# Optimization experiments

Measured on AMD Instinct MI355X. Metric: run time of the kernel, lower is better.

## Reference

```python
import jax, jax.numpy as jnp
import numpy as np

EPS = 1e-15
SCALING = 2.0  # softmax scaling in AttentionReference.forward default


def _psd(xs, mask):
    """ESPnet get_power_spectral_density_matrix with fused einsum.
    xs:   (B, F, C, T) complex64
    mask: (B, F, C, T) float32
    returns psd: (B, F, C, C) complex64
    """
    m = mask.mean(axis=-2)                               # (B, F, T)
    m = m / (m.sum(axis=-1, keepdims=True) + EPS)        # normalize over T
    # fused masked covariance: sum_t m[t] * x[:,t] x[:,t]^H
    return jnp.einsum('bfct,bft,bfet->bfce', xs, m.astype(xs.dtype), jnp.conj(xs))


def _attention_reference(psd_in, mlp_w, mlp_b, gvec_w, gvec_b):
    """AttentionReference.forward. psd_in: (B,F,C,C) complex -> u: (B,C)."""
    C = psd_in.shape[-1]
    eye = jnp.eye(C, dtype=bool)
    psd = jnp.where(eye, jnp.zeros((), psd_in.dtype), psd_in)   # zero diagonal
    psd = jnp.swapaxes(psd.sum(axis=-1) / (C - 1), -1, -2)      # (B, C, F)
    psd_feat = jnp.sqrt(psd.real ** 2 + psd.imag ** 2)          # (B, C, F)
    mlp = jnp.tanh(psd_feat @ mlp_w + mlp_b)                    # (B, C, A)
    e = (mlp @ gvec_w + gvec_b)[..., 0]                         # (B, C)
    return jax.nn.softmax(SCALING * e, axis=-1)                 # (B, C)


def _mvdr_vector(psd_s, psd_n, u):
    """get_mvdr_vector: ws = inv(psd_n) @ psd_s / trace(.) then contract with u."""
    numerator = jnp.linalg.inv(psd_n) @ psd_s                   # (B, F, C, C)
    trace = jnp.einsum('bfcc->bf', numerator)
    ws_mat = numerator / (trace[..., None, None] + EPS)
    return jnp.einsum('bfec,bc->bfe', ws_mat, u.astype(ws_mat.dtype))  # (B, F, C)


def setup_inputs() -> dict:
    key = jax.random.key(0)
    ks = jax.random.split(key, 6)
    B, T, C, F, A = 8, 512, 8, 257, 320
    return {
        'data_real': jax.random.normal(ks[0], (B, T, C, F), jnp.float32),
        'data_imag': jax.random.normal(ks[1], (B, T, C, F), jnp.float32),
        'mask_speech': jax.random.uniform(ks[2], (B, F, C, T), jnp.float32),
        'mask_noise': jax.random.uniform(ks[3], (B, F, C, T), jnp.float32),
        'mlp_w': jax.random.normal(ks[4], (F, A), jnp.float32) / np.sqrt(F),
        'mlp_b': jnp.zeros((A,), jnp.float32),
        'gvec_w': jax.random.normal(ks[5], (A, 1), jnp.float32) / np.sqrt(A),
        'gvec_b': jnp.zeros((1,), jnp.float32),
        'ilens': jnp.full((B,), T, dtype=jnp.int32),
    }


def reference(data_real, data_imag, mask_speech, mask_noise,
              mlp_w, mlp_b, gvec_w, gvec_b, ilens):
    # data: (B,T,C,F) -> permute(0,3,2,1) -> (B,F,C,T)
    data = jnp.transpose(data_real + 1j * data_imag, (0, 3, 2, 1)).astype(jnp.complex64)
    psd_speech = _psd(data, mask_speech)    # (B,F,C,C)
    psd_noise = _psd(data, mask_noise)      # (B,F,C,C)
    u = _attention_reference(psd_speech, mlp_w, mlp_b, gvec_w, gvec_b)  # (B,C)
    ws = _mvdr_vector(psd_speech, psd_noise, u)                         # (B,F,C)
    # apply_beamforming_vector: conj(ws) . data over channels -> (B,F,T)
    enhanced = jnp.einsum('bfc,bfct->bft', jnp.conj(ws), data)
    enhanced = jnp.swapaxes(enhanced, -1, -2)                           # (B,T,F)
    # complex output packed as real (B,T,F,2)
    return jnp.stack([enhanced.real, enhanced.imag], axis=-1)
```

## Files before the change

### kernel.cpp

```cpp
#include <hip/hip_runtime.h>
#include <math.h>

#define TTOT 512
#define CCH 8
#define FFR 257
#define AAH 320
#define NBF 2056
#define BF2 2112
#define NTIL 16
#define TTILE 32
#define EPSF 1e-15f
#define WSB (FFR * 8)

#define OFF_MBS 0
#define OFF_MBN (OFF_MBS + NBF * 512)
#define OFF_PART (OFF_MBN + NBF * 512)
#define OFF_PSDS (OFF_PART + NTIL * 256 * BF2)
#define OFF_PSDN (OFF_PSDS + NBF * 128)
#define OFF_E (OFF_PSDN + NBF * 128)
#define OFF_WS (OFF_E + 64)

__global__ __launch_bounds__(256) void k_mask(
    const float* __restrict__ mask_s, const float* __restrict__ mask_n,
    float* __restrict__ mbar_s, float* __restrict__ mbar_n) {
  int bf = blockIdx.x;
  int tid = threadIdx.x;
  int lane = tid & 63, wv = tid >> 6;
  const float2* ms = (const float2*)(mask_s + (size_t)bf * CCH * TTOT);
  const float2* mn = (const float2*)(mask_n + (size_t)bf * CCH * TTOT);
  float2 ss = make_float2(0.f, 0.f), sn = make_float2(0.f, 0.f);
#pragma unroll
  for (int c = 0; c < 8; ++c) {
    float2 a = ms[c * 256 + tid];
    ss.x += a.x; ss.y += a.y;
    float2 b = mn[c * 256 + tid];
    sn.x += b.x; sn.y += b.y;
  }
  float tots = ss.x + ss.y, totn = sn.x + sn.y;
#pragma unroll
  for (int off = 32; off > 0; off >>= 1) {
    tots += __shfl_down(tots, off);
    totn += __shfl_down(totn, off);
  }
  __shared__ float reds[4], redn[4];
  if (lane == 0) { reds[wv] = tots; redn[wv] = totn; }
  __syncthreads();
  float totS = reds[0] + reds[1] + reds[2] + reds[3];
  float totN = redn[0] + redn[1] + redn[2] + redn[3];
  float invs = 0.125f / (totS * 0.125f + EPSF);
  float invn = 0.125f / (totN * 0.125f + EPSF);
  ((float2*)(mbar_s + (size_t)bf * TTOT))[tid] = make_float2(ss.x * invs, ss.y * invs);
  ((float2*)(mbar_n + (size_t)bf * TTOT))[tid] = make_float2(sn.x * invn, sn.y * invn);
}

__global__ __launch_bounds__(256) void k_psd(
    const float* __restrict__ dr, const float* __restrict__ di,
    const float* __restrict__ mbar_s, const float* __restrict__ mbar_n,
    float* __restrict__ partial) {
  int lane = threadIdx.x & 63, wv = threadIdx.x >> 6;
  int bfb = blockIdx.x;
  int ttile = blockIdx.y;
  int bf = bfb * 64 + lane;
  if (bf > NBF - 1) bf = NBF - 1;
  int b = bf / FFR, f = bf - b * FFR;
  size_t dbase = (size_t)b * TTOT * CCH * FFR + f;
  int qi = (wv >> 1) * 4, qj = (wv & 1) * 4;
  bool diag = (qi == qj);
  int t0 = ttile * TTILE;

  float acc[16][4];
#pragma unroll
  for (int p = 0; p < 16; ++p) {
    acc[p][0] = 0.f; acc[p][1] = 0.f; acc[p][2] = 0.f; acc[p][3] = 0.f;
  }

#pragma unroll 2
  for (int tt = 0; tt < TTILE; ++tt) {
    int t = t0 + tt;
    const float* pr = dr + dbase + (size_t)t * (CCH * FFR);
    const float* pim_ = di + dbase + (size_t)t * (CCH * FFR);
    float ir[4], ii[4], jr[4], ji[4];
#pragma unroll
    for (int k = 0; k < 4; ++k) {
      ir[k] = pr[(qi + k) * FFR];
      ii[k] = pim_[(qi + k) * FFR];
    }
    if (!diag) {
#pragma unroll
      for (int k = 0; k < 4; ++k) {
        jr[k] = pr[(qj + k) * FFR];
        ji[k] = pim_[(qj + k) * FFR];
      }
    } else {
#pragma unroll
      for (int k = 0; k < 4; ++k) { jr[k] = ir[k]; ji[k] = ii[k]; }
    }
    float m_s = mbar_s[(size_t)bf * TTOT + t];
    float m_n = mbar_n[(size_t)bf * TTOT + t];
#pragma unroll
    for (int i4 = 0; i4 < 4; ++i4)
#pragma unroll
      for (int j4 = 0; j4 < 4; ++j4) {
        int p = i4 * 4 + j4;
        float pre = ir[i4] * jr[j4] + ii[i4] * ji[j4];
        float pimv = ii[i4] * jr[j4] - ir[i4] * ji[j4];
        acc[p][0] += m_s * pre; acc[p][1] += m_s * pimv;
        acc[p][2] += m_n * pre; acc[p][3] += m_n * pimv;
      }
  }

  size_t pbase = (size_t)ttile * 256 * BF2 + (size_t)wv * 64 * BF2 + bfb * 64 + lane;
#pragma unroll
  for (int p = 0; p < 16; ++p)
#pragma unroll
    for (int comp = 0; comp < 4; ++comp)
      partial[pbase + (size_t)(p * 4 + comp) * BF2] = acc[p][comp];
}

__global__ __launch_bounds__(256) void k_reduce(
    const float* __restrict__ partial, float* __restrict__ psd_s,
    float* __restrict__ psd_n) {
  int lane = threadIdx.x & 63, wv = threadIdx.x >> 6;
  int bfb = blockIdx.x;
  int g = blockIdx.y * 4 + wv;
  int bf = bfb * 64 + lane;
  const float* src = partial + (size_t)g * BF2 + bfb * 64 + lane;
  float s = 0.f;
#pragma unroll
  for (int nt = 0; nt < NTIL; ++nt) s += src[(size_t)nt * 256 * BF2];
  if (bf < NBF) {
    int w = g >> 6, rem = g & 63, p = rem >> 2, comp = rem & 3;
    int i = (w >> 1) * 4 + (p >> 2);
    int j = (w & 1) * 4 + (p & 3);
    float* dst = (comp < 2) ? psd_s : psd_n;
    dst[(size_t)bf * 128 + (i * 8 + j) * 2 + (comp & 1)] = s;
  }
}

__global__ __launch_bounds__(320) void k2_attn(
    const float* __restrict__ psd_s, const float* __restrict__ mlp_w,
    const float* __restrict__ mlp_b, const float* __restrict__ gvec_w,
    float* __restrict__ e_out) {
  __shared__ float feat[FFR];
  __shared__ float wred[5];
  int bx = blockIdx.x;
  int b = bx >> 3, c = bx & 7;
  int tid = threadIdx.x;
  int lane = tid & 63, wv = tid >> 6;
  if (tid < FFR) {
    const float* p = psd_s + (((size_t)(b * FFR + tid)) * 8 + c) * 16;
    float sre = 0.f, sim = 0.f;
#pragma unroll
    for (int e = 0; e < 8; ++e) {
      if (e != c) { sre += p[e * 2]; sim += p[e * 2 + 1]; }
    }
    sre *= (1.0f / 7.0f);
    sim *= (1.0f / 7.0f);
    feat[tid] = sqrtf(sre * sre + sim * sim);
  }
  __syncthreads();
  float acc = mlp_b[tid];
#pragma unroll 8
  for (int f = 0; f < FFR; ++f) acc += feat[f] * mlp_w[f * AAH + tid];
  float v = tanhf(acc) * gvec_w[tid];
#pragma unroll
  for (int off = 32; off > 0; off >>= 1) v += __shfl_down(v, off);
  if (lane == 0) wred[wv] = v;
  __syncthreads();
  if (tid == 0) e_out[bx] = wred[0] + wred[1] + wred[2] + wred[3] + wred[4];
}

__global__ __launch_bounds__(256) void k3_mvdr(
    const float* __restrict__ psd_s, const float* __restrict__ psd_n,
    const float* __restrict__ e_in, const float* __restrict__ gvec_b,
    float* __restrict__ ws) {
  int lane = threadIdx.x & 63, wv = threadIdx.x >> 6;
  int bf = blockIdx.x * 4 + wv;
  int b = bf / FFR;
  int r = lane >> 3, c = lane & 7;
  float2 n = ((const float2*)(psd_n + (size_t)bf * 128))[lane];
  float2 s = ((const float2*)(psd_s + (size_t)bf * 128))[lane];

#pragma unroll
  for (int k = 0; k < 8; ++k) {
    float pvre = __shfl(n.x, k * 9), pvim = __shfl(n.y, k * 9);
    float dinv = 1.f / (pvre * pvre + pvim * pvim);
    float pire = pvre * dinv, piim = -pvim * dinv;
    if (r == k) {
      float2 nn = n, ss = s;
      n.x = nn.x * pire - nn.y * piim; n.y = nn.x * piim + nn.y * pire;
      s.x = ss.x * pire - ss.y * piim; s.y = ss.x * piim + ss.y * pire;
    }
    float fre = __shfl(n.x, r * 8 + k), fim = __shfl(n.y, r * 8 + k);
    float pnre = __shfl(n.x, k * 8 + c), pnim = __shfl(n.y, k * 8 + c);
    float psre = __shfl(s.x, k * 8 + c), psim = __shfl(s.y, k * 8 + c);
    if (r != k) {
      n.x -= fre * pnre - fim * pnim; n.y -= fre * pnim + fim * pnre;
      s.x -= fre * psre - fim * psim; s.y -= fre * psim + fim * psre;
    }
  }
  float trx = (r == c) ? s.x : 0.f, tryy = (r == c) ? s.y : 0.f;
#pragma unroll
  for (int off = 1; off < 64; off <<= 1) {
    trx += __shfl_xor(trx, off);
    tryy += __shfl_xor(tryy, off);
  }
  float val = 2.f * (e_in[b * 8 + c] + gvec_b[0]);
  float mx = val;
#pragma unroll
  for (int off = 1; off < 8; off <<= 1) mx = fmaxf(mx, __shfl_xor(mx, off));
  float pe = expf(val - mx);
  float psum = pe;
#pragma unroll
  for (int off = 1; off < 8; off <<= 1) psum += __shfl_xor(psum, off);
  float uc = pe / psum;
  float wre = s.x * uc, wim = s.y * uc;
#pragma unroll
  for (int off = 1; off < 8; off <<= 1) {
    wre += __shfl_xor(wre, off);
    wim += __shfl_xor(wim, off);
  }
  float tre = trx + EPSF, tim = tryy;
  float d2 = 1.f / (tre * tre + tim * tim);
  float owre = (wre * tre + wim * tim) * d2;
  float owim = (wim * tre - wre * tim) * d2;
  if (c == 0) ((float2*)ws)[(size_t)bf * 8 + r] = make_float2(owre, owim);
}

__global__ __launch_bounds__(256) void k4_beam(
    const float* __restrict__ dr, const float* __restrict__ di,
    const float* __restrict__ ws, float* __restrict__ out) {
  __shared__ float2 wsp[FFR * 9];
  int b = blockIdx.y;
  int t0 = blockIdx.x * 4;
  int tid = threadIdx.x;
  const float2* wsg = (const float2*)ws + (size_t)b * WSB;
  for (int i = tid; i < FFR * 8; i += 256) {
    int f = i >> 3, c = i & 7;
    wsp[f * 9 + c] = wsg[i];
  }
  __syncthreads();
  for (int ts = 0; ts < 4; ++ts) {
    int t = t0 + ts;
    const float* drb = dr + (size_t)(b * TTOT + t) * (CCH * FFR);
    const float* dib = di + (size_t)(b * TTOT + t) * (CCH * FFR);
    for (int f = tid; f < FFR; f += 256) {
      float are = 0.f, aim = 0.f;
#pragma unroll
      for (int c = 0; c < 8; ++c) {
        float xre = drb[c * FFR + f];
        float xim = dib[c * FFR + f];
        float2 w = wsp[f * 9 + c];
        are += w.x * xre + w.y * xim;
        aim += w.x * xim - w.y * xre;
      }
      ((float2*)out)[(size_t)(b * TTOT + t) * FFR + f] = make_float2(are, aim);
    }
  }
}

extern "C" void kernel_launch(void* const* d_in, const int* in_sizes, int n_in,
                              void* d_out, int out_size, void* d_ws, size_t ws_size,
                              hipStream_t stream) {
  const float* dr = (const float*)d_in[0];
  const float* di = (const float*)d_in[1];
  const float* mask_s = (const float*)d_in[2];
  const float* mask_n = (const float*)d_in[3];
  const float* mlp_w = (const float*)d_in[4];
  const float* mlp_b = (const float*)d_in[5];
  const float* gvec_w = (const float*)d_in[6];
  const float* gvec_b = (const float*)d_in[7];
  float* out = (float*)d_out;

  float* wsf = (float*)d_ws;
  float* mbar_s = wsf + OFF_MBS;
  float* mbar_n = wsf + OFF_MBN;
  float* part = wsf + OFF_PART;
  float* psd_s = wsf + OFF_PSDS;
  float* psd_n = wsf + OFF_PSDN;
  float* e_arr = wsf + OFF_E;
  float* wsv = wsf + OFF_WS;

  hipLaunchKernelGGL(k_mask, dim3(NBF), dim3(256), 0, stream,
                     mask_s, mask_n, mbar_s, mbar_n);
  hipLaunchKernelGGL(k_psd, dim3(33, NTIL), dim3(256), 0, stream,
                     dr, di, mbar_s, mbar_n, part);
  hipLaunchKernelGGL(k_reduce, dim3(33, 64), dim3(256), 0, stream,
                     part, psd_s, psd_n);
  hipLaunchKernelGGL(k2_attn, dim3(64), dim3(320), 0, stream,
                     psd_s, mlp_w, mlp_b, gvec_w, e_arr);
  hipLaunchKernelGGL(k3_mvdr, dim3(514), dim3(256), 0, stream,
                     psd_s, psd_n, e_arr, gvec_b, wsv);
  hipLaunchKernelGGL(k4_beam, dim3(128, 8), dim3(256), 0, stream, dr, di, wsv, out);
}
```

Measured before the change: 296.6 us.

## Double-buffer PSD loads, stage masks in LDS, vectorize mask reduction

The PSD kernel now stages the per-tile mask weights into shared memory with float4 loads. It double-buffers the per-timestep channel loads in registers so global loads overlap the FMA work, and it drops the diagonal-wave load-skip branch. It also adds a launch-bounds occupancy hint. The mask kernel uses float4 loads with 128 threads per block instead of float2 with 256. The cost is more register pressure from two 16-float buffers plus 64 accumulators, and redundant loads on diagonal waves.

```diff
diff --git a/kernel.cpp b/kernel.cpp
--- a/kernel.cpp
+++ b/kernel.cpp
@@ -20,101 +20,128 @@
 #define OFF_E (OFF_PSDN + NBF * 128)
 #define OFF_WS (OFF_E + 64)
 
-__global__ __launch_bounds__(256) void k_mask(
+__global__ __launch_bounds__(128) void k_mask(
     const float* __restrict__ mask_s, const float* __restrict__ mask_n,
     float* __restrict__ mbar_s, float* __restrict__ mbar_n) {
   int bf = blockIdx.x;
   int tid = threadIdx.x;
   int lane = tid & 63, wv = tid >> 6;
-  const float2* ms = (const float2*)(mask_s + (size_t)bf * CCH * TTOT);
-  const float2* mn = (const float2*)(mask_n + (size_t)bf * CCH * TTOT);
-  float2 ss = make_float2(0.f, 0.f), sn = make_float2(0.f, 0.f);
+  const float4* ms = (const float4*)(mask_s + (size_t)bf * CCH * TTOT);
+  const float4* mn = (const float4*)(mask_n + (size_t)bf * CCH * TTOT);
+  float4 ss = make_float4(0.f, 0.f, 0.f, 0.f);
+  float4 sn = make_float4(0.f, 0.f, 0.f, 0.f);
 #pragma unroll
   for (int c = 0; c < 8; ++c) {
-    float2 a = ms[c * 256 + tid];
-    ss.x += a.x; ss.y += a.y;
-    float2 b = mn[c * 256 + tid];
-    sn.x += b.x; sn.y += b.y;
-  }
-  float tots = ss.x + ss.y, totn = sn.x + sn.y;
+    float4 a = ms[c * 128 + tid];
+    ss.x += a.x; ss.y += a.y; ss.z += a.z; ss.w += a.w;
+    float4 b = mn[c * 128 + tid];
+    sn.x += b.x; sn.y += b.y; sn.z += b.z; sn.w += b.w;
+  }
+  float tots = (ss.x + ss.y) + (ss.z + ss.w);
+  float totn = (sn.x + sn.y) + (sn.z + sn.w);
 #pragma unroll
   for (int off = 32; off > 0; off >>= 1) {
     tots += __shfl_down(tots, off);
     totn += __shfl_down(totn, off);
   }
-  __shared__ float reds[4], redn[4];
+  __shared__ float reds[2], redn[2];
   if (lane == 0) { reds[wv] = tots; redn[wv] = totn; }
   __syncthreads();
-  float totS = reds[0] + reds[1] + reds[2] + reds[3];
-  float totN = redn[0] + redn[1] + redn[2] + redn[3];
-  float invs = 0.125f / (totS * 0.125f + EPSF);
-  float invn = 0.125f / (totN * 0.125f + EPSF);
-  ((float2*)(mbar_s + (size_t)bf * TTOT))[tid] = make_float2(ss.x * invs, ss.y * invs);
-  ((float2*)(mbar_n + (size_t)bf * TTOT))[tid] = make_float2(sn.x * invn, sn.y * invn);
-}
-
-__global__ __launch_bounds__(256) void k_psd(
+  float invs = 0.125f / ((reds[0] + reds[1]) * 0.125f + EPSF);
+  float invn = 0.125f / ((redn[0] + redn[1]) * 0.125f + EPSF);
+  ((float4*)(mbar_s + (size_t)bf * TTOT))[tid] =
+      make_float4(ss.x * invs, ss.y * invs, ss.z * invs, ss.w * invs);
+  ((float4*)(mbar_n + (size_t)bf * TTOT))[tid] =
+      make_float4(sn.x * invn, sn.y * invn, sn.z * invn, sn.w * invn);
+}
+
+__global__ __launch_bounds__(256, 3) void k_psd(
     const float* __restrict__ dr, const float* __restrict__ di,
     const float* __restrict__ mbar_s, const float* __restrict__ mbar_n,
     float* __restrict__ partial) {
-  int lane = threadIdx.x & 63, wv = threadIdx.x >> 6;
-  int bfb = blockIdx.x;
-  int ttile = blockIdx.y;
-  int bf = bfb * 64 + lane;
-  if (bf > NBF - 1) bf = NBF - 1;
+  __shared__ float lms[64][33];
+  __shared__ float lmn[64][33];
+  int tid = threadIdx.x;
+  int lane = tid & 63, wv = tid >> 6;
+  int bfb = blockIdx.x, ttile = blockIdx.y;
+  int t0 = ttile * TTILE;
+
+  {
+    int bfi = tid >> 2;
+    int qo = (tid & 3) * 8;
+    int bfg = bfb * 64 + bfi; if (bfg > NBF - 1) bfg = NBF - 1;
+    const float* ps = mbar_s + (size_t)bfg * TTOT + t0 + qo;
+    const float* pn = mbar_n + (size_t)bfg * TTOT + t0 + qo;
+    float4 a = *(const float4*)ps;
+    float4 b = *(const float4*)(ps + 4);
+    float4 c = *(const float4*)pn;
+    float4 d = *(const float4*)(pn + 4);
+    lms[bfi][qo + 0] = a.x; lms[bfi][qo + 1] = a.y;
+    lms[bfi][qo + 2] = a.z; lms[bfi][qo + 3] = a.w;
+    lms[bfi][qo + 4] = b.x; lms[bfi][qo + 5] = b.y;
+    lms[bfi][qo + 6] = b.z; lms[bfi][qo + 7] = b.w;
+    lmn[bfi][qo + 0] = c.x; lmn[bfi][qo + 1] = c.y;
+    lmn[bfi][qo + 2] = c.z; lmn[bfi][qo + 3] = c.w;
+    lmn[bfi][qo + 4] = d.x; lmn[bfi][qo + 5] = d.y;
+    lmn[bfi][qo + 6] = d.z; lmn[bfi][qo + 7] = d.w;
+  }
+
+  int bf = bfb * 64 + lane; if (bf > NBF - 1) bf = NBF - 1;
   int b = bf / FFR, f = bf - b * FFR;
-  size_t dbase = (size_t)b * TTOT * CCH * FFR + f;
+  const float* br = dr + (size_t)b * TTOT * CCH * FFR + (size_t)t0 * CCH * FFR + f;
+  const float* bi = di + (size_t)b * TTOT * CCH * FFR + (size_t)t0 * CCH * FFR + f;
   int qi = (wv >> 1) * 4, qj = (wv & 1) * 4;
-  bool diag = (qi == qj);
-  int t0 = ttile * TTILE;
-
-  float acc[16][4];
-#pragma unroll
-  for (int p = 0; p < 16; ++p) {
-    acc[p][0] = 0.f; acc[p][1] = 0.f; acc[p][2] = 0.f; acc[p][3] = 0.f;
-  }
-
-#pragma unroll 2
-  for (int tt = 0; tt < TTILE; ++tt) {
-    int t = t0 + tt;
-    const float* pr = dr + dbase + (size_t)t * (CCH * FFR);
-    const float* pim_ = di + dbase + (size_t)t * (CCH * FFR);
-    float ir[4], ii[4], jr[4], ji[4];
-#pragma unroll
-    for (int k = 0; k < 4; ++k) {
-      ir[k] = pr[(qi + k) * FFR];
-      ii[k] = pim_[(qi + k) * FFR];
-    }
-    if (!diag) {
-#pragma unroll
-      for (int k = 0; k < 4; ++k) {
-        jr[k] = pr[(qj + k) * FFR];
-        ji[k] = pim_[(qj + k) * FFR];
-      }
-    } else {
-#pragma unroll
-      for (int k = 0; k < 4; ++k) { jr[k] = ir[k]; ji[k] = ii[k]; }
-    }
-    float m_s = mbar_s[(size_t)bf * TTOT + t];
-    float m_n = mbar_n[(size_t)bf * TTOT + t];
+  int ro[8];
+#pragma unroll
+  for (int k = 0; k < 4; ++k) { ro[k] = (qi + k) * FFR; ro[4 + k] = (qj + k) * FFR; }
+
+  float acc[64];
+#pragma unroll
+  for (int g = 0; g < 64; ++g) acc[g] = 0.f;
+
+  float A[16], B[16];
+
+  auto LOADX = [&](float (&buf)[16], int tt) {
+    const float* pr = br + (size_t)tt * (CCH * FFR);
+    const float* pi_ = bi + (size_t)tt * (CCH * FFR);
+#pragma unroll
+    for (int k = 0; k < 8; ++k) {
+      buf[k] = pr[ro[k]];
+      buf[8 + k] = pi_[ro[k]];
+    }
+  };
+  auto FMAX = [&](float (&buf)[16], int tt) {
+    float m_s = lms[lane][tt];
+    float m_n = lmn[lane][tt];
 #pragma unroll
     for (int i4 = 0; i4 < 4; ++i4)
 #pragma unroll
       for (int j4 = 0; j4 < 4; ++j4) {
         int p = i4 * 4 + j4;
-        float pre = ir[i4] * jr[j4] + ii[i4] * ji[j4];
-        float pimv = ii[i4] * jr[j4] - ir[i4] * ji[j4];
-        acc[p][0] += m_s * pre; acc[p][1] += m_s * pimv;
-        acc[p][2] += m_n * pre; acc[p][3] += m_n * pimv;
+        float pre = buf[i4] * buf[4 + j4] + buf[8 + i4] * buf[12 + j4];
+        float pim = buf[8 + i4] * buf[4 + j4] - buf[i4] * buf[12 + j4];
+        acc[p * 4 + 0] += m_s * pre;
+        acc[p * 4 + 1] += m_s * pim;
+        acc[p * 4 + 2] += m_n * pre;
+        acc[p * 4 + 3] += m_n * pim;
       }
-  }
-
-  size_t pbase = (size_t)ttile * 256 * BF2 + (size_t)wv * 64 * BF2 + bfb * 64 + lane;
-#pragma unroll
-  for (int p = 0; p < 16; ++p)
-#pragma unroll
-    for (int comp = 0; comp < 4; ++comp)
-      partial[pbase + (size_t)(p * 4 + comp) * BF2] = acc[p][comp];
+  };
+
+  LOADX(A, 0);
+  LOADX(B, 1);
+  __syncthreads();
+#pragma unroll
+  for (int tt = 0; tt < TTILE; tt += 2) {
+    FMAX(A, tt);
+    if (tt + 2 < TTILE) LOADX(A, tt + 2);
+    FMAX(B, tt + 1);
+    if (tt + 3 < TTILE) LOADX(B, tt + 3);
+  }
+
+  size_t pbase = ((size_t)ttile * 256 + wv * 64) * BF2 + bfb * 64 + lane;
+#pragma unroll
+  for (int g = 0; g < 64; ++g)
+    partial[pbase + (size_t)g * BF2] = acc[g];
 }
 
 __global__ __launch_bounds__(256) void k_reduce(
@@ -281,7 +308,7 @@
   float* e_arr = wsf + OFF_E;
   float* wsv = wsf + OFF_WS;
 
-  hipLaunchKernelGGL(k_mask, dim3(NBF), dim3(256), 0, stream,
+  hipLaunchKernelGGL(k_mask, dim3(NBF), dim3(128), 0, stream,
                      mask_s, mask_n, mbar_s, mbar_n);
   hipLaunchKernelGGL(k_psd, dim3(33, NTIL), dim3(256), 0, stream,
                      dr, di, mbar_s, mbar_n, part);
```

New measurement: 253.8 us. 14.4% less time.
